# Kernel optimization log

Measured on AMD Instinct MI355X. Metric: run time of the kernel, lower is better.

Reference implementation:

```python
import jax, jax.numpy as jnp
import numpy as np

B, C, H, W = 16, 256, 56, 56
NH = 8           # num_heads
BS = 8           # block_size
HALO = 3         # halo_size
WIN = BS + 2 * HALO   # 14
MLP = 4


def setup_inputs() -> dict:
    key = jax.random.key(0)
    ks = jax.random.split(key, 8)
    f = lambda k, shape, s: jax.random.normal(k, shape, jnp.float32) * s
    return dict(
        x=jax.random.normal(ks[0], (B, C, H, W), jnp.float32),
        ln1_g=jnp.ones((C,), jnp.float32), ln1_b=jnp.zeros((C,), jnp.float32),
        wq=f(ks[1], (C, C), C ** -0.5), bq=jnp.zeros((C,), jnp.float32),
        wkv=f(ks[2], (2 * C, C), C ** -0.5), bkv=jnp.zeros((2 * C,), jnp.float32),
        bias=f(ks[3], (1, NH, 1, BS * BS, WIN * WIN), 0.02),
        gamma1=jnp.full((1, C, 1, 1), 1e-6, jnp.float32),
        ln2_g=jnp.ones((C,), jnp.float32), ln2_b=jnp.zeros((C,), jnp.float32),
        w1=f(ks[4], (MLP * C, C), 0.02), b1=jnp.zeros((MLP * C,), jnp.float32),
        w2=f(ks[5], (C, MLP * C), 0.02), b2=jnp.zeros((C,), jnp.float32),
        gamma2=jnp.full((1, 1, 1, C), 1e-6, jnp.float32),
    )


def _ln2d(x, g, b, eps=1e-5):
    # LayerNorm over channel dim of NCHW
    mu = jnp.mean(x, axis=1, keepdims=True)
    var = jnp.mean((x - mu) ** 2, axis=1, keepdims=True)
    return (x - mu) * jax.lax.rsqrt(var + eps) * g[None, :, None, None] + b[None, :, None, None]


def _halo_attn(x, wq, bq, wkv, bkv, bias):
    Bn, Cc, Hh, Ww = x.shape
    dh = Cc // NH
    scale = dh ** -0.5
    nHb, nWb = Hh // BS, Ww // BS
    xh = jnp.transpose(x, (0, 2, 3, 1))            # B,H,W,C
    q = xh @ wq.T + bq                             # 1x1 conv
    kv = xh @ wkv.T + bkv                          # B,H,W,2C
    # q blocks: B,nh,nblocks,bs^2,dh
    q = q.reshape(Bn, nHb, BS, nWb, BS, NH, dh).transpose(0, 5, 1, 3, 2, 4, 6)
    q = q.reshape(Bn, NH, nHb * nWb, BS * BS, dh)
    # kv halo windows
    kvp = jnp.pad(kv, ((0, 0), (HALO, HALO), (HALO, HALO), (0, 0)))
    ih = (jnp.arange(nHb) * BS)[:, None] + jnp.arange(WIN)[None, :]
    iw = (jnp.arange(nWb) * BS)[:, None] + jnp.arange(WIN)[None, :]
    kvw = kvp[:, ih[:, None, :, None], iw[None, :, None, :], :]
    kvw = kvw.reshape(Bn, nHb * nWb, WIN * WIN, NH, 2 * dh).transpose(0, 3, 1, 2, 4)
    k, v = kvw[..., :dh], kvw[..., dh:]
    attn = jnp.einsum('bhnqd,bhnkd->bhnqk', q, k) * scale + bias
    attn = jax.nn.softmax(attn, axis=-1)
    out = jnp.einsum('bhnqk,bhnkd->bhnqd', attn, v)                   # B,nh,nb,bs^2,dh
    out = out.reshape(Bn, NH, nHb, nWb, BS, BS, dh).transpose(0, 1, 6, 2, 4, 3, 5)
    return out.reshape(Bn, Cc, Hh, Ww)


def _forward(x, ln1_g, ln1_b, wq, bq, wkv, bkv, bias, gamma1,
             ln2_g, ln2_b, w1, b1, w2, b2, gamma2):
    shortcut = x
    a = _halo_attn(_ln2d(x, ln1_g, ln1_b), wq, bq, wkv, bkv, bias)
    x = shortcut + gamma1 * a
    shortcut = x
    y = jnp.transpose(_ln2d(x, ln2_g, ln2_b), (0, 2, 3, 1))           # NHWC
    y = jax.nn.gelu(y @ w1.T + b1, approximate=False) @ w2.T + b2
    y = gamma2 * y
    return shortcut + jnp.transpose(y, (0, 3, 1, 2))


def reference(x, ln1_g, ln1_b, wq, bq, wkv, bkv, bias, gamma1,
              ln2_g, ln2_b, w1, b1, w2, b2, gamma2):
    return _forward(x, ln1_g, ln1_b, wq, bq, wkv, bkv, bias, gamma1,
                    ln2_g, ln2_b, w1, b1, w2, b2, gamma2)
```

## Files before the change

kernel.cpp:

```cpp
#include <hip/hip_runtime.h>
#include <hip/hip_bf16.h>
#include <math.h>

typedef unsigned short u16;
typedef float f32x4 __attribute__((ext_vector_type(4)));
typedef __bf16 bf16x8 __attribute__((ext_vector_type(8)));

__device__ __forceinline__ float bf2f(u16 u) {
    union { float f; unsigned int i; } v; v.i = ((unsigned int)u) << 16; return v.f;
}
__device__ __forceinline__ u16 f2bf(float f) {
    union { float f; unsigned int i; } v; v.f = f;
    unsigned int x = v.i;
    return (u16)((x + 0x7FFFu + ((x >> 16) & 1u)) >> 16);
}
__device__ __forceinline__ unsigned int cvt_pk_bf16(float lo, float hi) {
    unsigned int r;
    asm("v_cvt_pk_bf16_f32 %0, %1, %2" : "=v"(r) : "v"(lo), "v"(hi));
    return r;
}

__global__ __launch_bounds__(256) void k_prep(const float* __restrict__ wq, const float* __restrict__ wkv,
                                              const float* __restrict__ w1, const float* __restrict__ w2,
                                              u16* __restrict__ wqkvb, u16* __restrict__ w1p, u16* __restrict__ w2p) {
    const int bid = blockIdx.x, t = threadIdx.x;
    if (bid < 192) {
        int e = (bid * 256 + t) * 4;
        const float* src = (e < 65536) ? (wq + e) : (wkv + (e - 65536));
        float sc = (e < 65536) ? 0.17677669529663687f : 1.f;
        float4 v = *(const float4*)src;
        ushort4 o;
        o.x = f2bf(v.x * sc); o.y = f2bf(v.y * sc); o.z = f2bf(v.z * sc); o.w = f2bf(v.w * sc);
        *(ushort4*)(wqkvb + e) = o;
    } else if (bid < 320) {
        int tid = (bid - 192) * 256 + t;
        int kc = tid >> 11, rem = tid & 2047;
        int wave = rem >> 9, rem2 = rem & 511;
        int ks = rem2 >> 6, lane = rem2 & 63;
        int ln = lane & 15, quad = lane >> 4;
        const float* src = w1 + (size_t)(kc * 64 + wave * 16 + ln) * 256 + ks * 32 + quad * 8;
        float4 v0 = *(const float4*)src;
        float4 v1 = *(const float4*)(src + 4);
        alignas(16) u16 tmp[8];
        tmp[0] = f2bf(v0.x); tmp[1] = f2bf(v0.y); tmp[2] = f2bf(v0.z); tmp[3] = f2bf(v0.w);
        tmp[4] = f2bf(v1.x); tmp[5] = f2bf(v1.y); tmp[6] = f2bf(v1.z); tmp[7] = f2bf(v1.w);
        *(int4*)(w1p + (size_t)tid * 8) = *(int4*)tmp;
    } else {
        int tid = (bid - 320) * 256 + t;
        int kc = tid >> 11, rem = tid & 2047;
        int wave = rem >> 9, rem2 = rem & 511;
        int ks2 = rem2 >> 8, rem3 = rem2 & 255;
        int nt = rem3 >> 6, lane = rem3 & 63;
        int ln = lane & 15, quad = lane >> 4;
        const float* src = w2 + (size_t)(wave * 64 + nt * 16 + ln) * 1024 + kc * 64 + ks2 * 32 + quad * 8;
        float4 v0 = *(const float4*)src;
        float4 v1 = *(const float4*)(src + 4);
        alignas(16) u16 tmp[8];
        tmp[0] = f2bf(v0.x); tmp[1] = f2bf(v0.y); tmp[2] = f2bf(v0.z); tmp[3] = f2bf(v0.w);
        tmp[4] = f2bf(v1.x); tmp[5] = f2bf(v1.y); tmp[6] = f2bf(v1.z); tmp[7] = f2bf(v1.w);
        *(int4*)(w2p + (size_t)tid * 8) = *(int4*)tmp;
    }
}

__global__ __launch_bounds__(256) void k_transpose(const float* __restrict__ x, u16* __restrict__ xh) {
    __shared__ __align__(16) u16 tile[64][72];
    const int t = threadIdx.x;
    const int hw0 = blockIdx.x * 64;
    const int c0  = blockIdx.y * 64;
    const int b   = blockIdx.z;
    const int cl = t >> 2, wl = (t & 3) * 16;
    {
        int c = c0 + cl;
        const float* src = x + (size_t)(b * 256 + c) * 3136 + hw0 + wl;
        for (int q = 0; q < 4; q++) {
            float4 v = *(const float4*)(src + q * 4);
            u16* dst = &tile[cl][wl + q * 4];
            dst[0] = f2bf(v.x); dst[1] = f2bf(v.y); dst[2] = f2bf(v.z); dst[3] = f2bf(v.w);
        }
    }
    __syncthreads();
    const int hl = t >> 3, cl2 = (t & 7) * 8;
    for (int i = 0; i < 2; i++) {
        int hw = hl + i * 32;
        alignas(16) u16 tmp[8];
        for (int j = 0; j < 8; j++) tmp[j] = tile[cl2 + j][hw];
        u16* dst = xh + (size_t)(b * 3136 + hw0 + hw) * 256 + c0 + cl2;
        *(int4*)dst = *(int4*)tmp;
    }
}

__global__ __launch_bounds__(256) void k_ln(const u16* __restrict__ in, u16* __restrict__ out,
                                            const float* __restrict__ g, const float* __restrict__ bta) {
    const int wave = threadIdx.x >> 6, lane = threadIdx.x & 63;
    const int p = blockIdx.x * 4 + wave;
    ushort4 v = *(const ushort4*)(in + (size_t)p * 256 + lane * 4);
    float f0 = bf2f(v.x), f1 = bf2f(v.y), f2 = bf2f(v.z), f3 = bf2f(v.w);
    float s = f0 + f1 + f2 + f3;
    float sq = f0 * f0 + f1 * f1 + f2 * f2 + f3 * f3;
    for (int o = 32; o >= 1; o >>= 1) { s += __shfl_xor(s, o, 64); sq += __shfl_xor(sq, o, 64); }
    float m = s * (1.f / 256.f);
    float var = sq * (1.f / 256.f) - m * m;
    float inv = rsqrtf(var + 1e-5f);
    float4 gv = *(const float4*)(g + lane * 4);
    float4 bv = *(const float4*)(bta + lane * 4);
    ushort4 o4;
    o4.x = f2bf((f0 - m) * inv * gv.x + bv.x);
    o4.y = f2bf((f1 - m) * inv * gv.y + bv.y);
    o4.z = f2bf((f2 - m) * inv * gv.z + bv.z);
    o4.w = f2bf((f3 - m) * inv * gv.w + bv.w);
    *(ushort4*)(out + (size_t)p * 256 + lane * 4) = o4;
}

__global__ __launch_bounds__(256) void k_qkv(
    const u16* __restrict__ xn, const u16* __restrict__ Bw,
    const float* __restrict__ bq, const float* __restrict__ bkv,
    u16* __restrict__ out) {
    __shared__ __align__(16) u16 smem[17408];
    u16* As = smem;
    u16* Bs = smem + 4096;

    const int g = blockIdx.x;
    const int xcd = g & 7, idx = g >> 3;
    const int bm = xcd * 49 + idx / 6, bn = idx % 6;

    const int t = threadIdx.x;
    const int wave = t >> 6, lane = t & 63;
    const int wm = (wave >> 1) * 64, wn = (wave & 1) * 64;
    const int ln = lane & 15, quad = lane >> 4;

    f32x4 vzero = {0.f, 0.f, 0.f, 0.f};
    f32x4 acc[4][4];
    for (int i = 0; i < 4; i++) for (int j = 0; j < 4; j++) acc[i][j] = vzero;

    const int srow = t >> 2;
    const int scol = (t & 3) * 8;

    for (int k0 = 0; k0 < 256; k0 += 32) {
        for (int i = 0; i < 2; i++) {
            int r = srow + i * 64;
            *(int4*)&As[r * 32 + scol] = *(const int4*)(xn + (size_t)(bm * 128 + r) * 256 + k0 + scol);
            *(int4*)&Bs[r * 32 + scol] = *(const int4*)(Bw + (size_t)(bn * 128 + r) * 256 + k0 + scol);
        }
        __syncthreads();
        bf16x8 af[4], bfr[4];
        for (int mt = 0; mt < 4; mt++) af[mt] = *(const bf16x8*)&As[(wm + mt * 16 + ln) * 32 + quad * 8];
        for (int nt = 0; nt < 4; nt++) bfr[nt] = *(const bf16x8*)&Bs[(wn + nt * 16 + ln) * 32 + quad * 8];
        for (int mt = 0; mt < 4; mt++)
            for (int nt = 0; nt < 4; nt++)
                acc[mt][nt] = __builtin_amdgcn_mfma_f32_16x16x32_bf16(bfr[nt], af[mt], acc[mt][nt], 0, 0, 0);
        __syncthreads();
    }

    u16* Cs = smem;
    for (int nt = 0; nt < 4; nt++) {
        int gn0 = bn * 128 + wn + nt * 16 + quad * 4;
        f32x4 bv;
        if (gn0 < 256) {
            f32x4 tq = *(const f32x4*)(bq + gn0);
            bv = tq * 0.17677669529663687f;
        } else {
            bv = *(const f32x4*)(bkv + gn0 - 256);
        }
        for (int mt = 0; mt < 4; mt++) {
            ushort4 pk;
            pk.x = f2bf(acc[mt][nt][0] + bv[0]);
            pk.y = f2bf(acc[mt][nt][1] + bv[1]);
            pk.z = f2bf(acc[mt][nt][2] + bv[2]);
            pk.w = f2bf(acc[mt][nt][3] + bv[3]);
            *(ushort4*)&Cs[(wm + mt * 16 + ln) * 136 + wn + nt * 16 + quad * 4] = pk;
        }
    }
    __syncthreads();
    const int row = t >> 4, col = (t & 15) * 8;
    for (int pass = 0; pass < 8; pass++) {
        int rr = pass * 16 + row;
        int4 v = *(int4*)&Cs[rr * 136 + col];
        *(int4*)(out + (size_t)(bm * 128 + rr) * 768 + bn * 128 + col) = v;
    }
}

__global__ __launch_bounds__(256) void k_mlp(
    const u16* __restrict__ xn, const u16* __restrict__ x2,
    const u16* __restrict__ w1p, const float* __restrict__ b1,
    const u16* __restrict__ w2p, const float* __restrict__ b2,
    const float* __restrict__ g2v, float* __restrict__ outT) {
    __shared__ __align__(16) u16 smem[16896 + 2 * 8704];
    u16* As = smem;

    const int g = blockIdx.x;
    const int bm = (g & 7) * 98 + (g >> 3);

    const int t = threadIdx.x;
    const int wave = t >> 6, lane = t & 63;
    const int ln = lane & 15, quad = lane >> 4;
    const int wn64 = wave * 64;
    const int wq4 = (wave >> 1) * 4 + (wave & 1) * 2;

    f32x4 vzero = {0.f, 0.f, 0.f, 0.f};
    f32x4 acc[4][4];
    for (int i = 0; i < 4; i++) for (int j = 0; j < 4; j++) acc[i][j] = vzero;

    {
        const int srow = t >> 2, scb = (t & 3) * 8;
        for (int c = 0; c < 8; c++) {
            int col = scb + c * 32;
            *(int4*)&As[srow * 264 + col] = *(const int4*)(xn + (size_t)(bm * 64 + srow) * 256 + col);
        }
    }
    __syncthreads();

    for (int kc = 0; kc < 8; kc++) {
        u16* Hs = smem + 16896 + (kc & 1) * 8704;
        bf16x8 w1f[2][8];
        {
            const u16* w1b = w1p + (size_t)(kc * 8 + wq4) * 4096 + lane * 8;
            #pragma unroll
            for (int nt = 0; nt < 2; nt++)
                #pragma unroll
                for (int ks = 0; ks < 8; ks++)
                    w1f[nt][ks] = *(const bf16x8*)(w1b + nt * 4096 + ks * 512);
        }
        f32x4 up[4][2];
        #pragma unroll
        for (int i = 0; i < 4; i++) { up[i][0] = vzero; up[i][1] = vzero; }
        #pragma unroll
        for (int ks = 0; ks < 8; ks++) {
            #pragma unroll
            for (int mt = 0; mt < 4; mt++) {
                bf16x8 af = *(const bf16x8*)&As[(mt * 16 + ln) * 264 + ks * 32 + quad * 8];
                up[mt][0] = __builtin_amdgcn_mfma_f32_16x16x32_bf16(w1f[0][ks], af, up[mt][0], 0, 0, 0);
                up[mt][1] = __builtin_amdgcn_mfma_f32_16x16x32_bf16(w1f[1][ks], af, up[mt][1], 0, 0, 0);
            }
        }
        bf16x8 w2f[4][4];
        #pragma unroll
        for (int ks2 = 0; ks2 < 4; ks2++) {
            const u16* w2b = w2p + (size_t)((((kc * 2 + (ks2 >> 1)) * 4 + wave) * 2 + (ks2 & 1)) * 4) * 512 + lane * 8;
            #pragma unroll
            for (int nt = 0; nt < 4; nt++)
                w2f[ks2][nt] = *(const bf16x8*)(w2b + nt * 512);
        }
        #pragma unroll
        for (int nt = 0; nt < 2; nt++) {
            float4 bv = *(const float4*)(b1 + kc * 128 + wave * 32 + nt * 16 + quad * 4);
            #pragma unroll
            for (int mt = 0; mt < 4; mt++) {
                float v0 = up[mt][nt][0] + bv.x;
                float v1 = up[mt][nt][1] + bv.y;
                float v2 = up[mt][nt][2] + bv.z;
                float v3 = up[mt][nt][3] + bv.w;
                ushort4 pk;
                pk.x = f2bf(v0 * (1.f / (1.f + __expf(-1.702f * v0))));
                pk.y = f2bf(v1 * (1.f / (1.f + __expf(-1.702f * v1))));
                pk.z = f2bf(v2 * (1.f / (1.f + __expf(-1.702f * v2))));
                pk.w = f2bf(v3 * (1.f / (1.f + __expf(-1.702f * v3))));
                *(ushort4*)&Hs[(mt * 16 + ln) * 136 + wave * 32 + nt * 16 + quad * 4] = pk;
            }
        }
        __syncthreads();
        #pragma unroll
        for (int ks2 = 0; ks2 < 4; ks2++) {
            bf16x8 hf[4];
            #pragma unroll
            for (int mt = 0; mt < 4; mt++)
                hf[mt] = *(const bf16x8*)&Hs[(mt * 16 + ln) * 136 + ks2 * 32 + quad * 8];
            #pragma unroll
            for (int nt = 0; nt < 4; nt++) {
                #pragma unroll
                for (int mt = 0; mt < 4; mt++)
                    acc[mt][nt] = __builtin_amdgcn_mfma_f32_16x16x32_bf16(hf[mt], w2f[ks2][nt], acc[mt][nt], 0, 0, 0);
            }
        }
    }

    const int b = bm / 49;
    for (int nt = 0; nt < 4; nt++) {
        int gn = wn64 + nt * 16 + ln;
        float bs = b2[gn], g2 = g2v[gn];
        for (int mt = 0; mt < 4; mt++) {
            int gm0 = bm * 64 + mt * 16 + quad * 4;
            int hw0 = gm0 - b * 3136;
            f32x4 res;
            for (int r = 0; r < 4; r++)
                res[r] = bf2f(x2[(size_t)(gm0 + r) * 256 + gn]) + g2 * (acc[mt][nt][r] + bs);
            *(f32x4*)(outT + (size_t)(b * 256 + gn) * 3136 + hw0) = res;
        }
    }
}

__global__ __launch_bounds__(256, 4) void k_attn(
    const u16* __restrict__ qkv, const float* __restrict__ bias,
    const u16* __restrict__ xh, const float* __restrict__ gamma1,
    u16* __restrict__ x2) {
    __shared__ __align__(16) u16 Kl[208 * 40];
    __shared__ __align__(16) u16 Vt[32 * 236];

    const int t = threadIdx.x;
    const int blk = blockIdx.x, head = blockIdx.y, b = blockIdx.z;
    const int bh = blk / 7, bw = blk - bh * 7;
    const int wave = t >> 6, lane = t & 63;
    const int ln = lane & 15, quad = lane >> 4;

    for (int cid = t; cid < 208 * 8; cid += 256) {
        int pos = cid >> 3, part = cid & 7;
        int i = pos / 14, j = pos - i * 14;
        int gh = bh * 8 - 3 + i, gw = bw * 8 - 3 + j;
        bool valid = (pos < 196) && ((unsigned)gh < 56u) && ((unsigned)gw < 56u);
        int d0 = (part & 3) * 8;
        int4 v = {0, 0, 0, 0};
        if (valid) {
            size_t p = (size_t)(b * 56 + gh) * 56 + gw;
            v = *(const int4*)(qkv + p * 768 + 256 + head * 64 + ((part & 4) ? 32 : 0) + d0);
        }
        if (!(part & 4)) {
            *(int4*)&Kl[pos * 40 + d0] = v;
        } else {
            alignas(16) u16 tmp[8];
            *(int4*)tmp = v;
            for (int jj = 0; jj < 8; jj++) Vt[(d0 + jj) * 236 + pos] = tmp[jj];
        }
    }
    __syncthreads();

    const int qrow = wave * 16 + ln;
    const int qh = bh * 8 + (qrow >> 3), qw = bw * 8 + (qrow & 7);
    const size_t qp = (size_t)(b * 56 + qh) * 56 + qw;
    bf16x8 qf = *(const bf16x8*)(qkv + qp * 768 + head * 32 + quad * 8);

    f32x4 s[13];
    const float* bp = bias + (size_t)(head * 64 + qrow) * 196 + quad * 4;
    #pragma unroll
    for (int nt = 0; nt < 13; nt++) {
        bf16x8 kf = *(const bf16x8*)&Kl[(nt * 16 + ln) * 40 + quad * 8];
        f32x4 c;
        if (nt < 12 || quad == 0) {
            c = *(const f32x4*)(bp + nt * 16);
        } else {
            c = (f32x4){-1e30f, -1e30f, -1e30f, -1e30f};
        }
        s[nt] = __builtin_amdgcn_mfma_f32_16x16x32_bf16(kf, qf, c, 0, 0, 0);
    }

    float mx = -1e30f;
    #pragma unroll
    for (int nt = 0; nt < 13; nt++)
        #pragma unroll
        for (int r = 0; r < 4; r++) mx = fmaxf(mx, s[nt][r]);
    mx = fmaxf(mx, __shfl_xor(mx, 16, 64));
    mx = fmaxf(mx, __shfl_xor(mx, 32, 64));
    float sum = 0.f;
    #pragma unroll
    for (int nt = 0; nt < 13; nt++)
        #pragma unroll
        for (int r = 0; r < 4; r++) {
            float e = __expf(s[nt][r] - mx);
            s[nt][r] = e;
            sum += e;
        }
    sum += __shfl_xor(sum, 16, 64);
    sum += __shfl_xor(sum, 32, 64);
    float rinv = 1.f / sum;

    unsigned int pk[13][2];
    #pragma unroll
    for (int nt = 0; nt < 13; nt++) {
        pk[nt][0] = cvt_pk_bf16(s[nt][0], s[nt][1]);
        pk[nt][1] = cvt_pk_bf16(s[nt][2], s[nt][3]);
    }

    f32x4 vzero = {0.f, 0.f, 0.f, 0.f};
    f32x4 o_acc[2];
    o_acc[0] = vzero; o_acc[1] = vzero;
    #pragma unroll
    for (int kc = 0; kc < 7; kc++) {
        union { int4 i4; bf16x8 v; } pu;
        pu.i4.x = pk[2 * kc][0];
        pu.i4.y = pk[2 * kc][1];
        pu.i4.z = (kc < 6) ? pk[2 * kc + 1][0] : 0;
        pu.i4.w = (kc < 6) ? pk[2 * kc + 1][1] : 0;
        #pragma unroll
        for (int n2 = 0; n2 < 2; n2++) {
            union { int4 i4; bf16x8 v; } vu;
            const u16* vb = &Vt[(n2 * 16 + ln) * 236 + kc * 32 + quad * 4];
            *(int2*)&vu.i4.x = *(const int2*)vb;
            if (kc < 6) {
                *(int2*)&vu.i4.z = *(const int2*)(vb + 16);
            } else {
                vu.i4.z = 0; vu.i4.w = 0;
            }
            o_acc[n2] = __builtin_amdgcn_mfma_f32_16x16x32_bf16(pu.v, vu.v, o_acc[n2], 0, 0, 0);
        }
    }

    float rr4[4];
    #pragma unroll
    for (int r = 0; r < 4; r++) rr4[r] = __shfl(rinv, quad * 4 + r, 16);

    #pragma unroll
    for (int n2 = 0; n2 < 2; n2++) {
        int c = head * 32 + n2 * 16 + ln;
        float g1 = gamma1[c];
        #pragma unroll
        for (int r = 0; r < 4; r++) {
            int q = wave * 16 + quad * 4 + r;
            int hh = bh * 8 + (q >> 3), ww = bw * 8 + (q & 7);
            size_t p = (size_t)(b * 56 + hh) * 56 + ww;
            float a = o_acc[n2][r] * rr4[r];
            x2[p * 256 + c] = f2bf(bf2f(xh[p * 256 + c]) + g1 * a);
        }
    }
}

extern "C" void kernel_launch(void* const* d_in, const int* in_sizes, int n_in,
                              void* d_out, int out_size, void* d_ws, size_t ws_size,
                              hipStream_t stream) {
    const float* x      = (const float*)d_in[0];
    const float* ln1_g  = (const float*)d_in[1];
    const float* ln1_b  = (const float*)d_in[2];
    const float* wq     = (const float*)d_in[3];
    const float* bq     = (const float*)d_in[4];
    const float* wkv    = (const float*)d_in[5];
    const float* bkv    = (const float*)d_in[6];
    const float* bias   = (const float*)d_in[7];
    const float* gamma1 = (const float*)d_in[8];
    const float* ln2_g  = (const float*)d_in[9];
    const float* ln2_b  = (const float*)d_in[10];
    const float* w1     = (const float*)d_in[11];
    const float* b1     = (const float*)d_in[12];
    const float* w2     = (const float*)d_in[13];
    const float* b2     = (const float*)d_in[14];
    const float* gamma2 = (const float*)d_in[15];

    char* ws = (char*)d_ws;
    u16* qkv   = (u16*)ws;
    u16* xh    = (u16*)(ws + 77070336);
    u16* x2    = (u16*)(ws + 102760448);
    u16* wqkvb = (u16*)(ws + 128450560);
    u16* w1p   = (u16*)(ws + 128843776);
    u16* w2p   = (u16*)(ws + 129368064);
    u16* xn1   = x2;
    u16* xn2   = xh;

    k_prep<<<dim3(448), 256, 0, stream>>>(wq, wkv, w1, w2, wqkvb, w1p, w2p);
    k_transpose<<<dim3(49, 4, 16), 256, 0, stream>>>(x, xh);
    k_ln<<<dim3(12544), 256, 0, stream>>>(xh, xn1, ln1_g, ln1_b);
    k_qkv<<<dim3(2352), 256, 0, stream>>>(xn1, wqkvb, bq, bkv, qkv);
    k_attn<<<dim3(49, 8, 16), 256, 0, stream>>>(qkv, bias, xh, gamma1, x2);
    k_ln<<<dim3(12544), 256, 0, stream>>>(x2, xn2, ln2_g, ln2_b);
    k_mlp<<<dim3(784), 256, 0, stream>>>(xn2, x2, w1p, b1, w2p, b2, gamma2, (float*)d_out);
}
```

Before: 335.4 us.

## Stream MLP A-operand from global into registers, drop LDS staging, raise occupancy

The MLP kernel no longer stages the 64x256 normalized input tile in shared memory. Each wave now reads its A fragments straight from global memory into a double-buffered register set, one k-step ahead. The W1 fragment load is split into two halves to cut register use, and launch bounds now ask for 3 blocks per CU. The smaller LDS footprint and register count aim to raise occupancy. In exchange, every wave re-reads the A tile from global/L2 on each of the 8 kc iterations, and the wq4 mapping changes to wave*2.

```diff
diff --git a/kernel.cpp b/kernel.cpp
--- a/kernel.cpp
+++ b/kernel.cpp
@@ -179,13 +179,12 @@
     }
 }
 
-__global__ __launch_bounds__(256) void k_mlp(
+__global__ __launch_bounds__(256, 3) void k_mlp(
     const u16* __restrict__ xn, const u16* __restrict__ x2,
     const u16* __restrict__ w1p, const float* __restrict__ b1,
     const u16* __restrict__ w2p, const float* __restrict__ b2,
     const float* __restrict__ g2v, float* __restrict__ outT) {
-    __shared__ __align__(16) u16 smem[16896 + 2 * 8704];
-    u16* As = smem;
+    __shared__ __align__(16) u16 smem[2 * 8704];
 
     const int g = blockIdx.x;
     const int bm = (g & 7) * 98 + (g >> 3);
@@ -194,42 +193,57 @@
     const int wave = t >> 6, lane = t & 63;
     const int ln = lane & 15, quad = lane >> 4;
     const int wn64 = wave * 64;
-    const int wq4 = (wave >> 1) * 4 + (wave & 1) * 2;
+    const int wq4 = wave * 2;
 
     f32x4 vzero = {0.f, 0.f, 0.f, 0.f};
     f32x4 acc[4][4];
     for (int i = 0; i < 4; i++) for (int j = 0; j < 4; j++) acc[i][j] = vzero;
 
-    {
-        const int srow = t >> 2, scb = (t & 3) * 8;
-        for (int c = 0; c < 8; c++) {
-            int col = scb + c * 32;
-            *(int4*)&As[srow * 264 + col] = *(const int4*)(xn + (size_t)(bm * 64 + srow) * 256 + col);
-        }
-    }
-    __syncthreads();
+    const u16* aB0 = xn + (size_t)(bm * 64 + ln) * 256 + quad * 8;
+    const u16* aB1 = aB0 + 16 * 256;
+    const u16* aB2 = aB0 + 32 * 256;
+    const u16* aB3 = aB0 + 48 * 256;
 
     for (int kc = 0; kc < 8; kc++) {
-        u16* Hs = smem + 16896 + (kc & 1) * 8704;
-        bf16x8 w1f[2][8];
-        {
-            const u16* w1b = w1p + (size_t)(kc * 8 + wq4) * 4096 + lane * 8;
+        u16* Hs = smem + (kc & 1) * 8704;
+        f32x4 up[4][2];
+        #pragma unroll
+        for (int i = 0; i < 4; i++) { up[i][0] = vzero; up[i][1] = vzero; }
+
+        bf16x8 af[2][4];
+        af[0][0] = *(const bf16x8*)(aB0);
+        af[0][1] = *(const bf16x8*)(aB1);
+        af[0][2] = *(const bf16x8*)(aB2);
+        af[0][3] = *(const bf16x8*)(aB3);
+
+        #pragma unroll
+        for (int h = 0; h < 2; h++) {
+            bf16x8 w1f[2][4];
+            {
+                const u16* w1b = w1p + (size_t)(kc * 8 + wq4) * 4096 + lane * 8 + h * 2048;
+                #pragma unroll
+                for (int nt = 0; nt < 2; nt++)
+                    #pragma unroll
+                    for (int k4 = 0; k4 < 4; k4++)
+                        w1f[nt][k4] = *(const bf16x8*)(w1b + nt * 4096 + k4 * 512);
+            }
             #pragma unroll
-            for (int nt = 0; nt < 2; nt++)
+            for (int k4 = 0; k4 < 4; k4++) {
+                const int ks = h * 4 + k4;
+                if (ks < 7) {
+                    const int nb = (ks + 1) & 1;
+                    const int off = (ks + 1) * 32;
+                    af[nb][0] = *(const bf16x8*)(aB0 + off);
+                    af[nb][1] = *(const bf16x8*)(aB1 + off);
+                    af[nb][2] = *(const bf16x8*)(aB2 + off);
+                    af[nb][3] = *(const bf16x8*)(aB3 + off);
+                }
+                const int cb = ks & 1;
                 #pragma unroll
-                for (int ks = 0; ks < 8; ks++)
-                    w1f[nt][ks] = *(const bf16x8*)(w1b + nt * 4096 + ks * 512);
-        }
-        f32x4 up[4][2];
-        #pragma unroll
-        for (int i = 0; i < 4; i++) { up[i][0] = vzero; up[i][1] = vzero; }
-        #pragma unroll
-        for (int ks = 0; ks < 8; ks++) {
-            #pragma unroll
-            for (int mt = 0; mt < 4; mt++) {
-                bf16x8 af = *(const bf16x8*)&As[(mt * 16 + ln) * 264 + ks * 32 + quad * 8];
-                up[mt][0] = __builtin_amdgcn_mfma_f32_16x16x32_bf16(w1f[0][ks], af, up[mt][0], 0, 0, 0);
-                up[mt][1] = __builtin_amdgcn_mfma_f32_16x16x32_bf16(w1f[1][ks], af, up[mt][1], 0, 0, 0);
+                for (int mt = 0; mt < 4; mt++) {
+                    up[mt][0] = __builtin_amdgcn_mfma_f32_16x16x32_bf16(w1f[0][k4], af[cb][mt], up[mt][0], 0, 0, 0);
+                    up[mt][1] = __builtin_amdgcn_mfma_f32_16x16x32_bf16(w1f[1][k4], af[cb][mt], up[mt][1], 0, 0, 0);
+                }
             }
         }
         bf16x8 w2f[4][4];
```

Result: slower. 458.4 us (+36.7%).
